# Kernel optimization log

Hardware: AMD Instinct MI355X
Metric: run time of the kernel (lower is better)

Reference implementation:

```python
import jax, jax.numpy as jnp
import numpy as np

EPS = 1e-08
B, ATT, RELA = 16, 64, 128
RNN, HID = 1024, 512


def setup_inputs() -> dict:
    key = jax.random.key(0)
    k = jax.random.split(key, 8)
    obj_vecs_e = jax.random.normal(k[0], (B, ATT, RNN), dtype=jnp.float32)
    rela_feats = jax.random.normal(k[1], (B, RELA, RNN), dtype=jnp.float32)
    p_rela_feats = jax.random.normal(k[2], (B, RELA, HID), dtype=jnp.float32)
    obj_rela_masks = jax.random.randint(k[3], (B, ATT, RELA), 0, 2, dtype=jnp.int32)
    # learned params: obj2att Linear(RNN -> HID), alpha_net Linear(HID -> 1)
    W_obj = jax.random.normal(k[4], (RNN, HID), dtype=jnp.float32) / np.sqrt(RNN)
    b_obj = jax.random.normal(k[5], (HID,), dtype=jnp.float32) * 0.01
    w_alpha = jax.random.normal(k[6], (HID,), dtype=jnp.float32) / np.sqrt(HID)
    b_alpha = jax.random.normal(k[7], (), dtype=jnp.float32) * 0.01
    return {
        "obj_vecs_e": obj_vecs_e,
        "rela_feats": rela_feats,
        "p_rela_feats": p_rela_feats,
        "W_obj": W_obj,
        "b_obj": b_obj,
        "w_alpha": w_alpha,
        "b_alpha": b_alpha,
        "obj_rela_masks": obj_rela_masks,
    }


def reference(obj_vecs_e, rela_feats, p_rela_feats, W_obj, b_obj, w_alpha, b_alpha, obj_rela_masks):
    # att_obj: [B, ATT, HID]
    att_obj = jnp.einsum("bad,dh->bah", obj_vecs_e, W_obj) + b_obj
    # broadcast add: [B, ATT, RELA, HID]
    dot = jnp.tanh(p_rela_feats[:, None, :, :] + att_obj[:, :, None, :])
    # alpha_net: scores [B, ATT, RELA]
    scores = jnp.einsum("barh,h->bar", dot, w_alpha) + b_alpha
    weight = jax.nn.softmax(scores, axis=-1)
    mask = obj_rela_masks.astype(weight.dtype)
    weight = weight * mask
    weight = weight / (jnp.sum(weight, axis=-1, keepdims=True) + EPS)
    # weighted sum of relation features: [B, ATT, RNN]
    att_res = jnp.einsum("bar,brd->bad", weight, rela_feats)
    return att_res
```

## Files before the change

kernel.cpp:

```cpp
#include <hip/hip_runtime.h>


constexpr int B_   = 16;
constexpr int ATT  = 64;
constexpr int RELA = 128;
constexpr int RNN  = 1024;
constexpr int HID  = 512;
constexpr int M_   = B_ * ATT;
constexpr float EPS_ = 1e-8f;
constexpr float K2LN = 2.885390081777927f;
constexpr int RT  = 8;
constexpr int NRT = RELA / RT;
constexpr int HG  = 64;
constexpr int NHG = HID / HG;
constexpr int HW  = 16;

typedef short bf16x8 __attribute__((ext_vector_type(8)));
typedef float f32x4  __attribute__((ext_vector_type(4)));

__device__ __forceinline__ unsigned short f2bf(float f) {
    unsigned u = __float_as_uint(f);
    u += 0x7FFFu + ((u >> 16) & 1u);
    return (unsigned short)(u >> 16);
}

__global__ __launch_bounds__(256) void k0_precast(const float* __restrict__ A,
                                                  const float* __restrict__ W,
                                                  unsigned short* __restrict__ Abf,
                                                  unsigned short* __restrict__ WT) {
    const int bid = blockIdx.x;
    const int tid = threadIdx.x;
    if (bid < 512) {
        const size_t idx = ((size_t)bid * 256 + tid) << 3;
        const float4 f0 = *reinterpret_cast<const float4*>(&A[idx]);
        const float4 f1 = *reinterpret_cast<const float4*>(&A[idx + 4]);
        unsigned short us[8] = {f2bf(f0.x), f2bf(f0.y), f2bf(f0.z), f2bf(f0.w),
                                f2bf(f1.x), f2bf(f1.y), f2bf(f1.z), f2bf(f1.w)};
        *reinterpret_cast<uint4*>(&Abf[idx]) = *reinterpret_cast<uint4*>(us);
    } else {
        __shared__ float Ts[64][68];
        const int wb = bid - 512;
        const int k0 = (wb >> 3) << 6, n0 = (wb & 7) << 6;
        #pragma unroll
        for (int i = 0; i < 4; ++i) {
            const int r = (tid >> 4) + (i << 4);
            const int c4 = (tid & 15) << 2;
            *reinterpret_cast<float4*>(&Ts[r][c4]) =
                *reinterpret_cast<const float4*>(&W[(size_t)(k0 + r) * HID + n0 + c4]);
        }
        __syncthreads();
        const int n = tid >> 2, kq = (tid & 3) << 4;
        unsigned short us[16];
        #pragma unroll
        for (int e = 0; e < 16; ++e)
            us[e] = f2bf(Ts[kq + e][n]);
        unsigned short* dst = &WT[(size_t)(n0 + n) * RNN + k0 + kq];
        *reinterpret_cast<uint4*>(dst)     = *reinterpret_cast<uint4*>(us);
        *reinterpret_cast<uint4*>(dst + 8) = *reinterpret_cast<uint4*>(us + 8);
    }
}

__global__ __launch_bounds__(256) void k1_mfma(const unsigned short* __restrict__ Abf,
                                               const unsigned short* __restrict__ WT,
                                               const float* __restrict__ b_obj,
                                               float* __restrict__ att_obj) {
    const int tid = threadIdx.x;
    const int lane = tid & 63;
    const int wave = tid >> 6;
    const int m0 = (blockIdx.x << 5) + ((wave >> 1) << 4);
    const int n0 = (blockIdx.y << 5) + ((wave & 1) << 4);
    const int row  = lane & 15;
    const int koff = (lane >> 4) << 3;
    const unsigned short* ap = &Abf[(size_t)(m0 + row) * RNN + koff];
    const unsigned short* bp = &WT[(size_t)(n0 + row) * RNN + koff];
    f32x4 acc0 = {}, acc1 = {};
    #pragma unroll 4
    for (int k = 0; k < RNN; k += 64) {
        const bf16x8 a0 = *reinterpret_cast<const bf16x8*>(ap + k);
        const bf16x8 b0 = *reinterpret_cast<const bf16x8*>(bp + k);
        const bf16x8 a1 = *reinterpret_cast<const bf16x8*>(ap + k + 32);
        const bf16x8 b1 = *reinterpret_cast<const bf16x8*>(bp + k + 32);
        acc0 = __builtin_amdgcn_mfma_f32_16x16x32_bf16(a0, b0, acc0, 0, 0, 0);
        acc1 = __builtin_amdgcn_mfma_f32_16x16x32_bf16(a1, b1, acc1, 0, 0, 0);
    }
    const int dcol = lane & 15;
    const int drow0 = (lane >> 4) << 2;
    const float bias = b_obj[n0 + dcol];
    #pragma unroll
    for (int v = 0; v < 4; ++v)
        att_obj[(size_t)(m0 + drow0 + v) * HID + n0 + dcol] = (acc0[v] + acc1[v] + bias) * K2LN;
}

__global__ __launch_bounds__(256, 6) void k2a_scores(const float* __restrict__ att_obj,
                                                     const float* __restrict__ p_rela,
                                                     const float* __restrict__ w_alpha,
                                                     float* __restrict__ partials) {
    const int b  = blockIdx.x;
    const int rt = blockIdx.y;
    const int hg = blockIdx.z;
    const int tid = threadIdx.x;
    const int lane = tid & 63;
    const int wave = tid >> 6;

    __shared__ float ps[RT][HG];
    __shared__ float red[4][RT][ATT];

    if (tid < 128) {
        const int row = tid >> 4, c4 = (tid & 15) << 2;
        float4 v = *reinterpret_cast<const float4*>(
            &p_rela[((size_t)b * RELA + rt * RT + row) * HID + hg * HG + c4]);
        v.x *= K2LN; v.y *= K2LN; v.z *= K2LN; v.w *= K2LN;
        *reinterpret_cast<float4*>(&ps[row][c4]) = v;
    }
    const int hbase = hg * HG + wave * HW;
    float4 q[4], wa[4];
    #pragma unroll
    for (int i = 0; i < 4; ++i) {
        q[i]  = *reinterpret_cast<const float4*>(&att_obj[(size_t)((b << 6) + lane) * HID + hbase + (i << 2)]);
        wa[i] = *reinterpret_cast<const float4*>(&w_alpha[hbase + (i << 2)]);
    }
    __syncthreads();

    float acc[RT] = {};
    #pragma unroll
    for (int i = 0; i < 4; ++i) {
        const float qq[4] = {q[i].x, q[i].y, q[i].z, q[i].w};
        const float ww[4] = {2.f * wa[i].x, 2.f * wa[i].y, 2.f * wa[i].z, 2.f * wa[i].w};
        #pragma unroll
        for (int r = 0; r < RT; ++r) {
            const float4 p4 = *reinterpret_cast<const float4*>(&ps[r][wave * HW + (i << 2)]);
            const float pp[4] = {p4.x, p4.y, p4.z, p4.w};
            #pragma unroll
            for (int j = 0; j < 4; ++j) {
                const float e = __builtin_amdgcn_exp2f(pp[j] + qq[j]);
                acc[r] = fmaf(ww[j], __builtin_amdgcn_rcpf(e + 1.f), acc[r]);
            }
        }
    }

    #pragma unroll
    for (int r = 0; r < RT; ++r)
        red[wave][r][lane] = acc[r];
    __syncthreads();

    const int a = tid & 63, rg = tid >> 6;
    float2 o;
    o.x = red[0][rg * 2][a] + red[1][rg * 2][a] + red[2][rg * 2][a] + red[3][rg * 2][a];
    o.y = red[0][rg * 2 + 1][a] + red[1][rg * 2 + 1][a] + red[2][rg * 2 + 1][a] + red[3][rg * 2 + 1][a];
    const size_t ba = (size_t)(b << 6) + a;
    *reinterpret_cast<float2*>(&partials[(ba * NHG + hg) * RELA + rt * RT + rg * 2]) = o;
}

__global__ __launch_bounds__(256) void k2b_softmax(const float* __restrict__ partials,
                                                   const int* __restrict__ masks,
                                                   float* __restrict__ weight) {
    const int tid = threadIdx.x;
    const int lane = tid & 63;
    const int wave = tid >> 6;
    const int ba = (blockIdx.x << 2) + wave;

    const float* pp = &partials[(size_t)ba * NHG * RELA];
    float s0 = 0.f, s1 = 0.f;
    #pragma unroll
    for (int hs = 0; hs < NHG; ++hs) {
        s0 += pp[hs * RELA + lane];
        s1 += pp[hs * RELA + lane + 64];
    }
    s0 = -s0; s1 = -s1;

    float m = fmaxf(s0, s1);
    #pragma unroll
    for (int off = 32; off > 0; off >>= 1)
        m = fmaxf(m, __shfl_xor(m, off));
    const float e0 = __expf(s0 - m), e1 = __expf(s1 - m);
    float sum = e0 + e1;
    #pragma unroll
    for (int off = 32; off > 0; off >>= 1)
        sum += __shfl_xor(sum, off);
    const float inv = 1.f / sum;
    const float m0 = (float)masks[(size_t)ba * RELA + lane];
    const float m1 = (float)masks[(size_t)ba * RELA + lane + 64];
    const float w0 = e0 * inv * m0;
    const float w1 = e1 * inv * m1;
    float ms = w0 + w1;
    #pragma unroll
    for (int off = 32; off > 0; off >>= 1)
        ms += __shfl_xor(ms, off);
    const float inv2 = 1.f / (ms + EPS_);
    weight[(size_t)ba * RELA + lane]      = w0 * inv2;
    weight[(size_t)ba * RELA + lane + 64] = w1 * inv2;
}

__global__ __launch_bounds__(256) void k3_wsum(const float* __restrict__ weight,
                                               const float* __restrict__ rela,
                                               float* __restrict__ out) {
    const int b = blockIdx.x;
    const int d_base = blockIdx.y << 6;
    const int tid = threadIdx.x;
    const int col = tid & 15;
    const int a0 = (tid >> 4) << 2;

    __shared__ float ws_s[ATT][132];
    __shared__ float rs[32 * 64];
    #pragma unroll
    for (int i = 0; i < 8; ++i) {
        const int fi = tid + (i << 8);
        const int a = fi >> 5, r0 = (fi & 31) << 2;
        *reinterpret_cast<float4*>(&ws_s[a][r0]) =
            *reinterpret_cast<const float4*>(&weight[((size_t)b * ATT + a) * RELA + r0]);
    }
    float4 acc[4] = {};
    for (int rc = 0; rc < 4; ++rc) {
        __syncthreads();
        #pragma unroll
        for (int i = 0; i < 2; ++i) {
            const int fi = tid + (i << 8);
            const int rr = fi >> 4, c = fi & 15;
            *reinterpret_cast<float4*>(&rs[(rr << 6) + (c << 2)]) =
                *reinterpret_cast<const float4*>(&rela[((size_t)b * RELA + (rc << 5) + rr) * RNN + d_base + (c << 2)]);
        }
        __syncthreads();
        #pragma unroll 8
        for (int rr = 0; rr < 32; ++rr) {
            const float4 x = *reinterpret_cast<const float4*>(&rs[(rr << 6) + (col << 2)]);
            const int r = (rc << 5) + rr;
            #pragma unroll
            for (int ai = 0; ai < 4; ++ai) {
                const float wv = ws_s[a0 + ai][r];
                acc[ai].x = fmaf(wv, x.x, acc[ai].x);
                acc[ai].y = fmaf(wv, x.y, acc[ai].y);
                acc[ai].z = fmaf(wv, x.z, acc[ai].z);
                acc[ai].w = fmaf(wv, x.w, acc[ai].w);
            }
        }
    }
    #pragma unroll
    for (int ai = 0; ai < 4; ++ai)
        *reinterpret_cast<float4*>(&out[((size_t)(b << 6) + a0 + ai) * RNN + d_base + (col << 2)]) = acc[ai];
}

extern "C" void kernel_launch(void* const* d_in, const int* in_sizes, int n_in,
                              void* d_out, int out_size, void* d_ws, size_t ws_size,
                              hipStream_t stream) {
    const float* obj_vecs = (const float*)d_in[0];
    const float* rela     = (const float*)d_in[1];
    const float* p_rela   = (const float*)d_in[2];
    const float* W_obj    = (const float*)d_in[3];
    const float* b_obj    = (const float*)d_in[4];
    const float* w_alpha  = (const float*)d_in[5];
    const int*   masks    = (const int*)d_in[7];
    float* out = (float*)d_out;

    char* ws = (char*)d_ws;
    unsigned short* Abf = (unsigned short*)(ws);
    unsigned short* WT  = (unsigned short*)(ws + (2u << 20));
    float* att_obj      = (float*)(ws + (3u << 20));
    float* partials     = (float*)(ws + (5u << 20));
    float* weight       = (float*)(ws + (9u << 20));

    k0_precast<<<dim3(640), 256, 0, stream>>>(obj_vecs, W_obj, Abf, WT);
    k1_mfma<<<dim3(M_ / 32, HID / 32), 256, 0, stream>>>(Abf, WT, b_obj, att_obj);
    k2a_scores<<<dim3(B_, NRT, NHG), 256, 0, stream>>>(att_obj, p_rela, w_alpha, partials);
    k2b_softmax<<<dim3(M_ / 4), 256, 0, stream>>>(partials, masks, weight);
    k3_wsum<<<dim3(B_, RNN / 64), 256, 0, stream>>>(weight, rela, out);
}
```

Measured before the change: 54.82 us.

## Factor tanh exponent into precomputed products and fuse softmax into weighted sum

Precomputes exp2 of scaled p_rela in the precast kernel and exp2 of att_obj in the GEMM epilogue, so the inner score loop uses a multiply instead of an exp per (a,r,h) element. The softmax kernel is merged into the weighted-sum kernel, which removes one launch and the weight buffer round trip, though each block recomputes the softmax for its batch. It also stages w_alpha in shared memory, raises the k2a occupancy hint, and reuses workspace regions. Products of exponentials may overflow to inf for large inputs, where rcp still gives the correct limit but precision near the extremes can differ.

```diff
diff --git a/kernel.cpp b/kernel.cpp
--- a/kernel.cpp
+++ b/kernel.cpp
@@ -24,10 +24,12 @@
     return (unsigned short)(u >> 16);
 }
 
-__global__ __launch_bounds__(256) void k0_precast(const float* __restrict__ A,
-                                                  const float* __restrict__ W,
-                                                  unsigned short* __restrict__ Abf,
-                                                  unsigned short* __restrict__ WT) {
+__global__ __launch_bounds__(256) void k0_pre(const float* __restrict__ A,
+                                              const float* __restrict__ W,
+                                              const float* __restrict__ p_rela,
+                                              unsigned short* __restrict__ Abf,
+                                              unsigned short* __restrict__ WT,
+                                              float* __restrict__ Ep) {
     const int bid = blockIdx.x;
     const int tid = threadIdx.x;
     if (bid < 512) {
@@ -37,7 +39,7 @@
         unsigned short us[8] = {f2bf(f0.x), f2bf(f0.y), f2bf(f0.z), f2bf(f0.w),
                                 f2bf(f1.x), f2bf(f1.y), f2bf(f1.z), f2bf(f1.w)};
         *reinterpret_cast<uint4*>(&Abf[idx]) = *reinterpret_cast<uint4*>(us);
-    } else {
+    } else if (bid < 640) {
         __shared__ float Ts[64][68];
         const int wb = bid - 512;
         const int k0 = (wb >> 3) << 6, n0 = (wb & 7) << 6;
@@ -57,13 +59,27 @@
         unsigned short* dst = &WT[(size_t)(n0 + n) * RNN + k0 + kq];
         *reinterpret_cast<uint4*>(dst)     = *reinterpret_cast<uint4*>(us);
         *reinterpret_cast<uint4*>(dst + 8) = *reinterpret_cast<uint4*>(us + 8);
+    } else {
+        const size_t idx = ((size_t)(bid - 640) * 256 + tid) << 3;
+        float4 f0 = *reinterpret_cast<const float4*>(&p_rela[idx]);
+        float4 f1 = *reinterpret_cast<const float4*>(&p_rela[idx + 4]);
+        f0.x = __builtin_amdgcn_exp2f(f0.x * K2LN);
+        f0.y = __builtin_amdgcn_exp2f(f0.y * K2LN);
+        f0.z = __builtin_amdgcn_exp2f(f0.z * K2LN);
+        f0.w = __builtin_amdgcn_exp2f(f0.w * K2LN);
+        f1.x = __builtin_amdgcn_exp2f(f1.x * K2LN);
+        f1.y = __builtin_amdgcn_exp2f(f1.y * K2LN);
+        f1.z = __builtin_amdgcn_exp2f(f1.z * K2LN);
+        f1.w = __builtin_amdgcn_exp2f(f1.w * K2LN);
+        *reinterpret_cast<float4*>(&Ep[idx])     = f0;
+        *reinterpret_cast<float4*>(&Ep[idx + 4]) = f1;
     }
 }
 
 __global__ __launch_bounds__(256) void k1_mfma(const unsigned short* __restrict__ Abf,
                                                const unsigned short* __restrict__ WT,
                                                const float* __restrict__ b_obj,
-                                               float* __restrict__ att_obj) {
+                                               float* __restrict__ Eq) {
     const int tid = threadIdx.x;
     const int lane = tid & 63;
     const int wave = tid >> 6;
@@ -88,11 +104,12 @@
     const float bias = b_obj[n0 + dcol];
     #pragma unroll
     for (int v = 0; v < 4; ++v)
-        att_obj[(size_t)(m0 + drow0 + v) * HID + n0 + dcol] = (acc0[v] + acc1[v] + bias) * K2LN;
-}
-
-__global__ __launch_bounds__(256, 6) void k2a_scores(const float* __restrict__ att_obj,
-                                                     const float* __restrict__ p_rela,
+        Eq[(size_t)(m0 + drow0 + v) * HID + n0 + dcol] =
+            __builtin_amdgcn_exp2f((acc0[v] + acc1[v] + bias) * K2LN);
+}
+
+__global__ __launch_bounds__(256, 8) void k2a_scores(const float* __restrict__ Eq,
+                                                     const float* __restrict__ Ep,
                                                      const float* __restrict__ w_alpha,
                                                      float* __restrict__ partials) {
     const int b  = blockIdx.x;
@@ -103,36 +120,39 @@
     const int wave = tid >> 6;
 
     __shared__ float ps[RT][HG];
+    __shared__ float wws[HG];
     __shared__ float red[4][RT][ATT];
 
     if (tid < 128) {
         const int row = tid >> 4, c4 = (tid & 15) << 2;
-        float4 v = *reinterpret_cast<const float4*>(
-            &p_rela[((size_t)b * RELA + rt * RT + row) * HID + hg * HG + c4]);
-        v.x *= K2LN; v.y *= K2LN; v.z *= K2LN; v.w *= K2LN;
-        *reinterpret_cast<float4*>(&ps[row][c4]) = v;
+        *reinterpret_cast<float4*>(&ps[row][c4]) =
+            *reinterpret_cast<const float4*>(&Ep[((size_t)b * RELA + rt * RT + row) * HID + hg * HG + c4]);
+    } else if (tid < 144) {
+        const int c4 = (tid - 128) << 2;
+        float4 w = *reinterpret_cast<const float4*>(&w_alpha[hg * HG + c4]);
+        w.x *= 2.f; w.y *= 2.f; w.z *= 2.f; w.w *= 2.f;
+        *reinterpret_cast<float4*>(&wws[c4]) = w;
     }
     const int hbase = hg * HG + wave * HW;
-    float4 q[4], wa[4];
+    float4 eq[4];
+    #pragma unroll
+    for (int i = 0; i < 4; ++i)
+        eq[i] = *reinterpret_cast<const float4*>(&Eq[(size_t)((b << 6) + lane) * HID + hbase + (i << 2)]);
+    __syncthreads();
+
+    float acc[RT] = {};
     #pragma unroll
     for (int i = 0; i < 4; ++i) {
-        q[i]  = *reinterpret_cast<const float4*>(&att_obj[(size_t)((b << 6) + lane) * HID + hbase + (i << 2)]);
-        wa[i] = *reinterpret_cast<const float4*>(&w_alpha[hbase + (i << 2)]);
-    }
-    __syncthreads();
-
-    float acc[RT] = {};
-    #pragma unroll
-    for (int i = 0; i < 4; ++i) {
-        const float qq[4] = {q[i].x, q[i].y, q[i].z, q[i].w};
-        const float ww[4] = {2.f * wa[i].x, 2.f * wa[i].y, 2.f * wa[i].z, 2.f * wa[i].w};
+        const float qq[4] = {eq[i].x, eq[i].y, eq[i].z, eq[i].w};
+        const float4 w4 = *reinterpret_cast<const float4*>(&wws[wave * HW + (i << 2)]);
+        const float ww[4] = {w4.x, w4.y, w4.z, w4.w};
         #pragma unroll
         for (int r = 0; r < RT; ++r) {
             const float4 p4 = *reinterpret_cast<const float4*>(&ps[r][wave * HW + (i << 2)]);
             const float pp[4] = {p4.x, p4.y, p4.z, p4.w};
             #pragma unroll
             for (int j = 0; j < 4; ++j) {
-                const float e = __builtin_amdgcn_exp2f(pp[j] + qq[j]);
+                const float e = pp[j] * qq[j];
                 acc[r] = fmaf(ww[j], __builtin_amdgcn_rcpf(e + 1.f), acc[r]);
             }
         }
@@ -151,64 +171,66 @@
     *reinterpret_cast<float2*>(&partials[(ba * NHG + hg) * RELA + rt * RT + rg * 2]) = o;
 }
 
-__global__ __launch_bounds__(256) void k2b_softmax(const float* __restrict__ partials,
-                                                   const int* __restrict__ masks,
-                                                   float* __restrict__ weight) {
+__global__ __launch_bounds__(256) void k3_softmax_wsum(const float* __restrict__ partials,
+                                                       const int* __restrict__ masks,
+                                                       const float* __restrict__ rela,
+                                                       float* __restrict__ out) {
+    const int b = blockIdx.x;
+    const int d_base = blockIdx.y << 6;
     const int tid = threadIdx.x;
     const int lane = tid & 63;
     const int wave = tid >> 6;
-    const int ba = (blockIdx.x << 2) + wave;
-
-    const float* pp = &partials[(size_t)ba * NHG * RELA];
-    float s0 = 0.f, s1 = 0.f;
-    #pragma unroll
-    for (int hs = 0; hs < NHG; ++hs) {
-        s0 += pp[hs * RELA + lane];
-        s1 += pp[hs * RELA + lane + 64];
-    }
-    s0 = -s0; s1 = -s1;
-
-    float m = fmaxf(s0, s1);
-    #pragma unroll
-    for (int off = 32; off > 0; off >>= 1)
-        m = fmaxf(m, __shfl_xor(m, off));
-    const float e0 = __expf(s0 - m), e1 = __expf(s1 - m);
-    float sum = e0 + e1;
-    #pragma unroll
-    for (int off = 32; off > 0; off >>= 1)
-        sum += __shfl_xor(sum, off);
-    const float inv = 1.f / sum;
-    const float m0 = (float)masks[(size_t)ba * RELA + lane];
-    const float m1 = (float)masks[(size_t)ba * RELA + lane + 64];
-    const float w0 = e0 * inv * m0;
-    const float w1 = e1 * inv * m1;
-    float ms = w0 + w1;
-    #pragma unroll
-    for (int off = 32; off > 0; off >>= 1)
-        ms += __shfl_xor(ms, off);
-    const float inv2 = 1.f / (ms + EPS_);
-    weight[(size_t)ba * RELA + lane]      = w0 * inv2;
-    weight[(size_t)ba * RELA + lane + 64] = w1 * inv2;
-}
-
-__global__ __launch_bounds__(256) void k3_wsum(const float* __restrict__ weight,
-                                               const float* __restrict__ rela,
-                                               float* __restrict__ out) {
-    const int b = blockIdx.x;
-    const int d_base = blockIdx.y << 6;
-    const int tid = threadIdx.x;
+
+    __shared__ float ws_s[ATT][132];
+    __shared__ float rs[32 * 64];
+
+    const int rr4 = (tid & 31) << 2;
+    const int abase = tid >> 5;
+    #pragma unroll
+    for (int ao = 0; ao < 8; ++ao) {
+        const int a = (ao << 3) + abase;
+        const float* pp = &partials[(size_t)((b << 6) + a) * NHG * RELA];
+        float4 s = {0.f, 0.f, 0.f, 0.f};
+        #pragma unroll
+        for (int hg = 0; hg < NHG; ++hg) {
+            const float4 v = *reinterpret_cast<const float4*>(&pp[hg * RELA + rr4]);
+            s.x += v.x; s.y += v.y; s.z += v.z; s.w += v.w;
+        }
+        float4 o;
+        o.x = -s.x; o.y = -s.y; o.z = -s.z; o.w = -s.w;
+        *reinterpret_cast<float4*>(&ws_s[a][rr4]) = o;
+    }
+    __syncthreads();
+
+    #pragma unroll 1
+    for (int aa = 0; aa < 16; ++aa) {
+        const int a = (wave << 4) + aa;
+        const float s0 = ws_s[a][lane], s1 = ws_s[a][lane + 64];
+        float m = fmaxf(s0, s1);
+        #pragma unroll
+        for (int off = 32; off > 0; off >>= 1)
+            m = fmaxf(m, __shfl_xor(m, off));
+        const float e0 = __expf(s0 - m), e1 = __expf(s1 - m);
+        float sum = e0 + e1;
+        #pragma unroll
+        for (int off = 32; off > 0; off >>= 1)
+            sum += __shfl_xor(sum, off);
+        const float inv = __builtin_amdgcn_rcpf(sum);
+        const float m0 = (float)masks[((size_t)(b << 6) + a) * RELA + lane];
+        const float m1 = (float)masks[((size_t)(b << 6) + a) * RELA + lane + 64];
+        const float w0 = e0 * inv * m0;
+        const float w1 = e1 * inv * m1;
+        float ms = w0 + w1;
+        #pragma unroll
+        for (int off = 32; off > 0; off >>= 1)
+            ms += __shfl_xor(ms, off);
+        const float inv2 = 1.f / (ms + EPS_);
+        ws_s[a][lane]      = w0 * inv2;
+        ws_s[a][lane + 64] = w1 * inv2;
+    }
+
     const int col = tid & 15;
     const int a0 = (tid >> 4) << 2;
-
-    __shared__ float ws_s[ATT][132];
-    __shared__ float rs[32 * 64];
-    #pragma unroll
-    for (int i = 0; i < 8; ++i) {
-        const int fi = tid + (i << 8);
-        const int a = fi >> 5, r0 = (fi & 31) << 2;
-        *reinterpret_cast<float4*>(&ws_s[a][r0]) =
-            *reinterpret_cast<const float4*>(&weight[((size_t)b * ATT + a) * RELA + r0]);
-    }
     float4 acc[4] = {};
     for (int rc = 0; rc < 4; ++rc) {
         __syncthreads();
@@ -254,13 +276,12 @@
     char* ws = (char*)d_ws;
     unsigned short* Abf = (unsigned short*)(ws);
     unsigned short* WT  = (unsigned short*)(ws + (2u << 20));
-    float* att_obj      = (float*)(ws + (3u << 20));
-    float* partials     = (float*)(ws + (5u << 20));
-    float* weight       = (float*)(ws + (9u << 20));
-
-    k0_precast<<<dim3(640), 256, 0, stream>>>(obj_vecs, W_obj, Abf, WT);
-    k1_mfma<<<dim3(M_ / 32, HID / 32), 256, 0, stream>>>(Abf, WT, b_obj, att_obj);
-    k2a_scores<<<dim3(B_, NRT, NHG), 256, 0, stream>>>(att_obj, p_rela, w_alpha, partials);
-    k2b_softmax<<<dim3(M_ / 4), 256, 0, stream>>>(partials, masks, weight);
-    k3_wsum<<<dim3(B_, RNN / 64), 256, 0, stream>>>(weight, rela, out);
-}
+    float* Ep           = (float*)(ws + (4u << 20));
+    float* Eq           = (float*)(ws + (8u << 20));
+    float* partials     = (float*)(ws);
+
+    k0_pre<<<dim3(1152), 256, 0, stream>>>(obj_vecs, W_obj, p_rela, Abf, WT, Ep);
+    k1_mfma<<<dim3(M_ / 32, HID / 32), 256, 0, stream>>>(Abf, WT, b_obj, Eq);
+    k2a_scores<<<dim3(B_, NRT, NHG), 256, 0, stream>>>(Eq, Ep, w_alpha, partials);
+    k3_softmax_wsum<<<dim3(B_, RNN / 64), 256, 0, stream>>>(partials, masks, rela, out);
+}
```

Result: slower. 60.39 us (+10.2%).

## Factor tanh exponent into precomputed exp terms and split weighted-sum over ATT halves

Applied to the files above, without the earlier changes.

The exponential is split as exp(2p)*exp(2q). exp(2q) is computed once in the GEMM epilogue and exp(2p) once per tile when staging into shared memory, so the inner loop of the scores kernel does a multiply instead of an exp2 per (a,r,h) element. The sign of the tanh identity is folded into w_alpha, pre-scaled by -2 and staged in shared memory, which removes the negation in softmax. The scores kernel's occupancy hint goes from 6 to 8. The weighted-sum kernel gets a second grid dimension over ATT halves to double its block count. Computing exp of unbounded sums separately can overflow to inf, which rcp maps to 0, so accuracy at extreme inputs is the risk.

```diff
diff --git a/kernel.cpp b/kernel.cpp
--- a/kernel.cpp
+++ b/kernel.cpp
@@ -24,10 +24,10 @@
     return (unsigned short)(u >> 16);
 }
 
-__global__ __launch_bounds__(256) void k0_precast(const float* __restrict__ A,
-                                                  const float* __restrict__ W,
-                                                  unsigned short* __restrict__ Abf,
-                                                  unsigned short* __restrict__ WT) {
+__global__ __launch_bounds__(256) void k0_pre(const float* __restrict__ A,
+                                              const float* __restrict__ W,
+                                              unsigned short* __restrict__ Abf,
+                                              unsigned short* __restrict__ WT) {
     const int bid = blockIdx.x;
     const int tid = threadIdx.x;
     if (bid < 512) {
@@ -63,7 +63,7 @@
 __global__ __launch_bounds__(256) void k1_mfma(const unsigned short* __restrict__ Abf,
                                                const unsigned short* __restrict__ WT,
                                                const float* __restrict__ b_obj,
-                                               float* __restrict__ att_obj) {
+                                               float* __restrict__ Eq) {
     const int tid = threadIdx.x;
     const int lane = tid & 63;
     const int wave = tid >> 6;
@@ -88,10 +88,11 @@
     const float bias = b_obj[n0 + dcol];
     #pragma unroll
     for (int v = 0; v < 4; ++v)
-        att_obj[(size_t)(m0 + drow0 + v) * HID + n0 + dcol] = (acc0[v] + acc1[v] + bias) * K2LN;
-}
-
-__global__ __launch_bounds__(256, 6) void k2a_scores(const float* __restrict__ att_obj,
+        Eq[(size_t)(m0 + drow0 + v) * HID + n0 + dcol] =
+            __builtin_amdgcn_exp2f((acc0[v] + acc1[v] + bias) * K2LN);
+}
+
+__global__ __launch_bounds__(256, 8) void k2a_scores(const float* __restrict__ Eq,
                                                      const float* __restrict__ p_rela,
                                                      const float* __restrict__ w_alpha,
                                                      float* __restrict__ partials) {
@@ -103,36 +104,44 @@
     const int wave = tid >> 6;
 
     __shared__ float ps[RT][HG];
+    __shared__ float wws[HG];
     __shared__ float red[4][RT][ATT];
 
     if (tid < 128) {
         const int row = tid >> 4, c4 = (tid & 15) << 2;
         float4 v = *reinterpret_cast<const float4*>(
             &p_rela[((size_t)b * RELA + rt * RT + row) * HID + hg * HG + c4]);
-        v.x *= K2LN; v.y *= K2LN; v.z *= K2LN; v.w *= K2LN;
+        v.x = __builtin_amdgcn_exp2f(v.x * K2LN);
+        v.y = __builtin_amdgcn_exp2f(v.y * K2LN);
+        v.z = __builtin_amdgcn_exp2f(v.z * K2LN);
+        v.w = __builtin_amdgcn_exp2f(v.w * K2LN);
         *reinterpret_cast<float4*>(&ps[row][c4]) = v;
+    } else if (tid < 144) {
+        const int c4 = (tid - 128) << 2;
+        float4 w = *reinterpret_cast<const float4*>(&w_alpha[hg * HG + c4]);
+        w.x *= -2.f; w.y *= -2.f; w.z *= -2.f; w.w *= -2.f;
+        *reinterpret_cast<float4*>(&wws[c4]) = w;
     }
     const int hbase = hg * HG + wave * HW;
-    float4 q[4], wa[4];
+    float4 eq[4];
+    #pragma unroll
+    for (int i = 0; i < 4; ++i)
+        eq[i] = *reinterpret_cast<const float4*>(&Eq[(size_t)((b << 6) + lane) * HID + hbase + (i << 2)]);
+    __syncthreads();
+
+    float acc[RT] = {};
     #pragma unroll
     for (int i = 0; i < 4; ++i) {
-        q[i]  = *reinterpret_cast<const float4*>(&att_obj[(size_t)((b << 6) + lane) * HID + hbase + (i << 2)]);
-        wa[i] = *reinterpret_cast<const float4*>(&w_alpha[hbase + (i << 2)]);
-    }
-    __syncthreads();
-
-    float acc[RT] = {};
-    #pragma unroll
-    for (int i = 0; i < 4; ++i) {
-        const float qq[4] = {q[i].x, q[i].y, q[i].z, q[i].w};
-        const float ww[4] = {2.f * wa[i].x, 2.f * wa[i].y, 2.f * wa[i].z, 2.f * wa[i].w};
+        const float qq[4] = {eq[i].x, eq[i].y, eq[i].z, eq[i].w};
+        const float4 w4 = *reinterpret_cast<const float4*>(&wws[wave * HW + (i << 2)]);
+        const float ww[4] = {w4.x, w4.y, w4.z, w4.w};
         #pragma unroll
         for (int r = 0; r < RT; ++r) {
             const float4 p4 = *reinterpret_cast<const float4*>(&ps[r][wave * HW + (i << 2)]);
             const float pp[4] = {p4.x, p4.y, p4.z, p4.w};
             #pragma unroll
             for (int j = 0; j < 4; ++j) {
-                const float e = __builtin_amdgcn_exp2f(pp[j] + qq[j]);
+                const float e = pp[j] * qq[j];
                 acc[r] = fmaf(ww[j], __builtin_amdgcn_rcpf(e + 1.f), acc[r]);
             }
         }
@@ -166,7 +175,6 @@
         s0 += pp[hs * RELA + lane];
         s1 += pp[hs * RELA + lane + 64];
     }
-    s0 = -s0; s1 = -s1;
 
     float m = fmaxf(s0, s1);
     #pragma unroll
@@ -196,20 +204,21 @@
                                                float* __restrict__ out) {
     const int b = blockIdx.x;
     const int d_base = blockIdx.y << 6;
+    const int ah = blockIdx.z;
     const int tid = threadIdx.x;
     const int col = tid & 15;
-    const int a0 = (tid >> 4) << 2;
-
-    __shared__ float ws_s[ATT][132];
+    const int la0 = (tid >> 4) << 1;
+
+    __shared__ float ws_s[32][132];
     __shared__ float rs[32 * 64];
     #pragma unroll
-    for (int i = 0; i < 8; ++i) {
+    for (int i = 0; i < 4; ++i) {
         const int fi = tid + (i << 8);
         const int a = fi >> 5, r0 = (fi & 31) << 2;
         *reinterpret_cast<float4*>(&ws_s[a][r0]) =
-            *reinterpret_cast<const float4*>(&weight[((size_t)b * ATT + a) * RELA + r0]);
-    }
-    float4 acc[4] = {};
+            *reinterpret_cast<const float4*>(&weight[((size_t)b * ATT + (ah << 5) + a) * RELA + r0]);
+    }
+    float4 acc[2] = {};
     for (int rc = 0; rc < 4; ++rc) {
         __syncthreads();
         #pragma unroll
@@ -225,8 +234,8 @@
             const float4 x = *reinterpret_cast<const float4*>(&rs[(rr << 6) + (col << 2)]);
             const int r = (rc << 5) + rr;
             #pragma unroll
-            for (int ai = 0; ai < 4; ++ai) {
-                const float wv = ws_s[a0 + ai][r];
+            for (int ai = 0; ai < 2; ++ai) {
+                const float wv = ws_s[la0 + ai][r];
                 acc[ai].x = fmaf(wv, x.x, acc[ai].x);
                 acc[ai].y = fmaf(wv, x.y, acc[ai].y);
                 acc[ai].z = fmaf(wv, x.z, acc[ai].z);
@@ -235,8 +244,9 @@
         }
     }
     #pragma unroll
-    for (int ai = 0; ai < 4; ++ai)
-        *reinterpret_cast<float4*>(&out[((size_t)(b << 6) + a0 + ai) * RNN + d_base + (col << 2)]) = acc[ai];
+    for (int ai = 0; ai < 2; ++ai)
+        *reinterpret_cast<float4*>(
+            &out[((size_t)(b << 6) + (ah << 5) + la0 + ai) * RNN + d_base + (col << 2)]) = acc[ai];
 }
 
 extern "C" void kernel_launch(void* const* d_in, const int* in_sizes, int n_in,
@@ -254,13 +264,13 @@
     char* ws = (char*)d_ws;
     unsigned short* Abf = (unsigned short*)(ws);
     unsigned short* WT  = (unsigned short*)(ws + (2u << 20));
-    float* att_obj      = (float*)(ws + (3u << 20));
+    float* Eq           = (float*)(ws + (3u << 20));
     float* partials     = (float*)(ws + (5u << 20));
     float* weight       = (float*)(ws + (9u << 20));
 
-    k0_precast<<<dim3(640), 256, 0, stream>>>(obj_vecs, W_obj, Abf, WT);
-    k1_mfma<<<dim3(M_ / 32, HID / 32), 256, 0, stream>>>(Abf, WT, b_obj, att_obj);
-    k2a_scores<<<dim3(B_, NRT, NHG), 256, 0, stream>>>(att_obj, p_rela, w_alpha, partials);
+    k0_pre<<<dim3(640), 256, 0, stream>>>(obj_vecs, W_obj, Abf, WT);
+    k1_mfma<<<dim3(M_ / 32, HID / 32), 256, 0, stream>>>(Abf, WT, b_obj, Eq);
+    k2a_scores<<<dim3(B_, NRT, NHG), 256, 0, stream>>>(Eq, p_rela, w_alpha, partials);
     k2b_softmax<<<dim3(M_ / 4), 256, 0, stream>>>(partials, masks, weight);
-    k3_wsum<<<dim3(B_, RNN / 64), 256, 0, stream>>>(weight, rela, out);
-}
+    k3_wsum<<<dim3(B_, RNN / 64, 2), 256, 0, stream>>>(weight, rela, out);
+}
```

Result: faster. 47.51 us (median of 3 runs) (-13.3%).
